# Kernel tuning notes

Measured on AMD Instinct MI355X. Metric: run time of the kernel, lower is better.

## Reference

```python
import jax, jax.numpy as jnp
import numpy as np

H = 20          # n_hidden
D_IN = 64       # max_len_input (encoder GRU input size)
VOCAB = 128     # decoder_dict_size
B = 8192
S = 128
MAX_DEC = 6


def _gru_cell(x, h, W_ih, W_hh, b_ih, b_hh):
    # PyTorch GRU cell: gates ordered [r, z, n]
    gi = x @ W_ih.T + b_ih
    gh = h @ W_hh.T + b_hh
    ir, iz, inn = jnp.split(gi, 3, axis=-1)
    hr, hz, hn = jnp.split(gh, 3, axis=-1)
    r = jax.nn.sigmoid(ir + hr)
    z = jax.nn.sigmoid(iz + hz)
    n = jnp.tanh(inn + r * hn)
    return (1.0 - z) * n + z * h


def setup_inputs() -> dict:
    key = jax.random.key(0)
    ks = jax.random.split(key, 32)
    s = 0.1
    p = {}
    p["x"] = jax.random.normal(ks[0], (B, S, D_IN), dtype=jnp.float32)
    # encoder GRU (2 layers)
    p["enc_Wih0"] = jax.random.normal(ks[1], (3 * H, D_IN)) * s
    p["enc_Whh0"] = jax.random.normal(ks[2], (3 * H, H)) * s
    p["enc_bih0"] = jax.random.normal(ks[3], (3 * H,)) * s
    p["enc_bhh0"] = jax.random.normal(ks[4], (3 * H,)) * s
    p["enc_Wih1"] = jax.random.normal(ks[5], (3 * H, H)) * s
    p["enc_Whh1"] = jax.random.normal(ks[6], (3 * H, H)) * s
    p["enc_bih1"] = jax.random.normal(ks[7], (3 * H,)) * s
    p["enc_bhh1"] = jax.random.normal(ks[8], (3 * H,)) * s
    # decoder GRU (2 layers, input size H)
    p["dec_Wih0"] = jax.random.normal(ks[9], (3 * H, H)) * s
    p["dec_Whh0"] = jax.random.normal(ks[10], (3 * H, H)) * s
    p["dec_bih0"] = jax.random.normal(ks[11], (3 * H,)) * s
    p["dec_bhh0"] = jax.random.normal(ks[12], (3 * H,)) * s
    p["dec_Wih1"] = jax.random.normal(ks[13], (3 * H, H)) * s
    p["dec_Whh1"] = jax.random.normal(ks[14], (3 * H, H)) * s
    p["dec_bih1"] = jax.random.normal(ks[15], (3 * H,)) * s
    p["dec_bhh1"] = jax.random.normal(ks[16], (3 * H,)) * s
    # embedding / attention / output heads
    p["emb"] = jax.random.normal(ks[17], (VOCAB, H)) * s
    p["q_W"] = jax.random.normal(ks[18], (H, H)) * s
    p["q_b"] = jax.random.normal(ks[19], (H,)) * s
    p["comb_W"] = jax.random.normal(ks[20], (H, 2 * H)) * s
    p["comb_b"] = jax.random.normal(ks[21], (H,)) * s
    p["out_W"] = jax.random.normal(ks[22], (VOCAB, H)) * s
    p["out_b"] = jax.random.normal(ks[23], (VOCAB,)) * s
    return p


def reference(x, enc_Wih0, enc_Whh0, enc_bih0, enc_bhh0,
              enc_Wih1, enc_Whh1, enc_bih1, enc_bhh1,
              dec_Wih0, dec_Whh0, dec_bih0, dec_bhh0,
              dec_Wih1, dec_Whh1, dec_bih1, dec_bhh1,
              emb, q_W, q_b, comb_W, comb_b, out_W, out_b):
    b = x.shape[0]
    h0 = jnp.zeros((b, H), x.dtype)
    h1 = jnp.zeros((b, H), x.dtype)

    def enc_step(carry, xt):
        c0, c1 = carry
        c0 = _gru_cell(xt, c0, enc_Wih0, enc_Whh0, enc_bih0, enc_bhh0)
        c1 = _gru_cell(c0, c1, enc_Wih1, enc_Whh1, enc_bih1, enc_bhh1)
        return (c0, c1), c1

    (h0, h1), enc_out = jax.lax.scan(enc_step, (h0, h1), jnp.swapaxes(x, 0, 1))
    encoded = jnp.swapaxes(enc_out, 0, 1)  # [B, S, H]

    vec_in = jnp.zeros((b,), dtype=jnp.int32)
    logits_list, attn_list = [], []
    d0, d1 = h0, h1  # hidden carried from encoder
    for _ in range(MAX_DEC):
        e = emb[vec_in]                                 # [B, H]
        d0 = _gru_cell(e, d0, dec_Wih0, dec_Whh0, dec_bih0, dec_bhh0)
        d1 = _gru_cell(d0, d1, dec_Wih1, dec_Whh1, dec_bih1, dec_bhh1)
        buf = d1                                        # decoder output at this step
        query = buf @ q_W.T + q_b                       # [B, H]
        scores = jnp.einsum('bh,bsh->bs', query, encoded)
        w = jax.nn.softmax(scores, axis=1)              # [B, S]
        a = jnp.einsum('bs,bsh->bh', w, encoded)        # attention context
        comb = jnp.concatenate([buf, a], axis=1) @ comb_W.T + comb_b
        logits = comb @ out_W.T + out_b                 # [B, VOCAB]
        logits_list.append(logits)
        attn_list.append(w)
        vec_in = jnp.argmax(logits, axis=1)
    vec_out = jnp.stack(logits_list, axis=1)            # [B, 6, VOCAB]
    hidden = jnp.stack([d0, d1], axis=0)                # [2, B, H]
    attention_weights = jnp.stack(attn_list, axis=0)    # [6, B, S]
    return vec_out, hidden, attention_weights
```

## Files before the change

### kernel.cpp

```cpp
#include <hip/hip_runtime.h>


#define HN 20
#define DIN 64
#define NVOCAB 128
#define NB 8192
#define NS 128
#define NDEC 6

#define HID_OFF (NB * NDEC * NVOCAB)
#define ATTN_OFF (HID_OFF + 2 * NB * HN)

__device__ __forceinline__ float sigf(float x) {
    return 1.0f / (1.0f + __expf(-x));
}

__global__ __launch_bounds__(512)
void enc_kernel(const float* __restrict__ x,
                const float* __restrict__ Wih0, const float* __restrict__ Whh0,
                const float* __restrict__ bih0, const float* __restrict__ bhh0,
                const float* __restrict__ Wih1, const float* __restrict__ Whh1,
                const float* __restrict__ bih1, const float* __restrict__ bhh1,
                float* __restrict__ enc, float* __restrict__ hf0,
                float* __restrict__ hf1)
{
    __shared__ __align__(16) float W0[60][68];
    __shared__ __align__(16) float U0[60][28];
    __shared__ __align__(16) float W1[60][28];
    __shared__ __align__(16) float U1[60][28];
    __shared__ float bi0[60], bh0[60], bi1[60], bh1[60];
    __shared__ __align__(16) float xs[2][8][68];
    __shared__ __align__(16) float h0s[8][24];
    __shared__ __align__(16) float h1s[8][24];
    __shared__ float gs[8][80];

    const int tid  = threadIdx.x;
    const int bloc = tid & 7;
    const int r    = tid >> 3;
    const int sb   = tid >> 6;
    const int si   = tid & 63;
    const int bid  = (int)blockIdx.x;
    const int gblk = (bid & 7) * 128 + (bid >> 3);
    const int b0   = gblk * 8;

    for (int idx = tid; idx < 60 * 64; idx += 512)
        W0[idx >> 6][idx & 63] = Wih0[idx];
    for (int idx = tid; idx < 60 * 20; idx += 512) {
        int rr = idx / 20, ii = idx % 20;
        U0[rr][ii] = Whh0[idx];
        W1[rr][ii] = Wih1[idx];
        U1[rr][ii] = Whh1[idx];
    }
    if (tid < 60) {
        bi0[tid] = bih0[tid]; bh0[tid] = bhh0[tid];
        bi1[tid] = bih1[tid]; bh1[tid] = bhh1[tid];
    }
    for (int idx = tid; idx < 8 * 24; idx += 512) {
        (&h0s[0][0])[idx] = 0.0f;
        (&h1s[0][0])[idx] = 0.0f;
    }
    xs[0][sb][si] = x[(b0 + sb) * (NS * DIN) + si];
    __syncthreads();

    int cur = 0;
    for (int t = 0; t < NS; ++t) {
        float pf = 0.0f;
        if (t + 1 < NS)
            pf = x[((b0 + sb) * NS + t + 1) * DIN + si];

        if (r < 60) {
            float ax = bi0[r], ah = bh0[r];
            #pragma unroll
            for (int i = 0; i < DIN; ++i) ax += W0[r][i] * xs[cur][bloc][i];
            #pragma unroll
            for (int i = 0; i < HN; ++i)  ah += U0[r][i] * h0s[bloc][i];
            if (r < 40) gs[bloc][r] = ax + ah;
            else { gs[bloc][r] = ax; gs[bloc][r + 20] = ah; }
        }
        __syncthreads();

        xs[cur ^ 1][sb][si] = pf;
        if (r < HN) {
            float rr = sigf(gs[bloc][r]);
            float z  = sigf(gs[bloc][20 + r]);
            float n  = tanhf(gs[bloc][40 + r] + rr * gs[bloc][60 + r]);
            float hnew = (1.0f - z) * n + z * h0s[bloc][r];
            h0s[bloc][r] = hnew;
            if (t == NS - 1) hf0[(b0 + bloc) * HN + r] = hnew;
        }
        __syncthreads();

        if (r < 60) {
            float ax = bi1[r], ah = bh1[r];
            #pragma unroll
            for (int i = 0; i < HN; ++i) ax += W1[r][i] * h0s[bloc][i];
            #pragma unroll
            for (int i = 0; i < HN; ++i) ah += U1[r][i] * h1s[bloc][i];
            if (r < 40) gs[bloc][r] = ax + ah;
            else { gs[bloc][r] = ax; gs[bloc][r + 20] = ah; }
        }
        __syncthreads();

        if (r < HN) {
            float rr = sigf(gs[bloc][r]);
            float z  = sigf(gs[bloc][20 + r]);
            float n  = tanhf(gs[bloc][40 + r] + rr * gs[bloc][60 + r]);
            float hnew = (1.0f - z) * n + z * h1s[bloc][r];
            h1s[bloc][r] = hnew;
            enc[(t * HN + r) * NB + b0 + bloc] = hnew;
            if (t == NS - 1) hf1[(b0 + bloc) * HN + r] = hnew;
        }
        __syncthreads();
        cur ^= 1;
    }
}

__global__ __launch_bounds__(512)
void dec_kernel(const float* __restrict__ dWih0, const float* __restrict__ dWhh0,
                const float* __restrict__ dbih0, const float* __restrict__ dbhh0,
                const float* __restrict__ dWih1, const float* __restrict__ dWhh1,
                const float* __restrict__ dbih1, const float* __restrict__ dbhh1,
                const float* __restrict__ emb,  const float* __restrict__ qW,
                const float* __restrict__ qb,   const float* __restrict__ combW,
                const float* __restrict__ combb, const float* __restrict__ outW,
                const float* __restrict__ outb,
                const float* __restrict__ enc, const float* __restrict__ hf0,
                const float* __restrict__ hf1, float* __restrict__ out)
{
    __shared__ __align__(16) float el[NS * 164];
    __shared__ float ssb[NS * 9];
    __shared__ float hd0[8][24], hd1[8][24];
    __shared__ float gsd[8][80];
    __shared__ float qs[8][24];
    __shared__ float combp[8][24];
    __shared__ float cxp[2][20][8];
    __shared__ float pm[8][8];
    __shared__ int   pi[8][8];
    __shared__ float Ms[8], Sv[8];
    __shared__ int   toks[8];

    const int tid  = threadIdx.x;
    const int bloc = tid & 7;
    const int r    = tid >> 3;
    const int wv   = tid >> 6;
    const int bid  = (int)blockIdx.x;
    const int gblk = (bid & 7) * 128 + (bid >> 3);
    const int b0   = gblk * 8;

    for (int idx = tid; idx < 8 * HN; idx += 512) {
        int bb = idx & 7, k = idx >> 3;
        hd0[bb][k] = hf0[(b0 + bb) * HN + k];
        hd1[bb][k] = hf1[(b0 + bb) * HN + k];
    }
    if (tid < 8) toks[tid] = 0;
    for (int idx = tid; idx < NS * HN * 2; idx += 512) {
        int tk = idx >> 1, q = idx & 1;
        int t = tk / HN, k = tk % HN;
        float4 v = *(const float4*)(enc + (size_t)tk * NB + b0 + 4 * q);
        *(float4*)(&el[t * 164 + k * 8 + 4 * q]) = v;
    }
    __syncthreads();

    for (int s = 0; s < NDEC; ++s) {
        if (r < 60) {
            const float* er = emb + toks[bloc] * HN;
            float ax = dbih0[r], ah = dbhh0[r];
            #pragma unroll
            for (int i = 0; i < HN; ++i) {
                ax += dWih0[r * HN + i] * er[i];
                ah += dWhh0[r * HN + i] * hd0[bloc][i];
            }
            if (r < 40) gsd[bloc][r] = ax + ah;
            else { gsd[bloc][r] = ax; gsd[bloc][r + 20] = ah; }
        }
        __syncthreads();
        if (r < HN) {
            float rr = sigf(gsd[bloc][r]);
            float z  = sigf(gsd[bloc][20 + r]);
            float n  = tanhf(gsd[bloc][40 + r] + rr * gsd[bloc][60 + r]);
            hd0[bloc][r] = (1.0f - z) * n + z * hd0[bloc][r];
        }
        __syncthreads();
        if (r < 60) {
            float ax = dbih1[r], ah = dbhh1[r];
            #pragma unroll
            for (int i = 0; i < HN; ++i) {
                ax += dWih1[r * HN + i] * hd0[bloc][i];
                ah += dWhh1[r * HN + i] * hd1[bloc][i];
            }
            if (r < 40) gsd[bloc][r] = ax + ah;
            else { gsd[bloc][r] = ax; gsd[bloc][r + 20] = ah; }
        }
        __syncthreads();
        if (r < HN) {
            float rr = sigf(gsd[bloc][r]);
            float z  = sigf(gsd[bloc][20 + r]);
            float n  = tanhf(gsd[bloc][40 + r] + rr * gsd[bloc][60 + r]);
            hd1[bloc][r] = (1.0f - z) * n + z * hd1[bloc][r];
        }
        __syncthreads();
        if (r < HN) {
            float a = qb[r];
            #pragma unroll
            for (int i = 0; i < HN; ++i) a += qW[r * HN + i] * hd1[bloc][i];
            qs[bloc][r] = a;
        } else if (r < 2 * HN) {
            int k = r - HN;
            float a = combb[k];
            #pragma unroll
            for (int i = 0; i < HN; ++i) a += combW[k * 2 * HN + i] * hd1[bloc][i];
            combp[bloc][k] = a;
        }
        __syncthreads();
        float s0 = 0.0f, s1 = 0.0f;
        #pragma unroll
        for (int k = 0; k < HN; ++k) {
            float q = qs[bloc][k];
            s0 += q * el[r * 164 + k * 8 + bloc];
            s1 += q * el[(64 + r) * 164 + k * 8 + bloc];
        }
        {
            float m = fmaxf(s0, s1);
            m = fmaxf(m, __shfl_xor(m, 8));
            m = fmaxf(m, __shfl_xor(m, 16));
            m = fmaxf(m, __shfl_xor(m, 32));
            if (((tid >> 3) & 7) == 0) pm[wv][bloc] = m;
        }
        __syncthreads();
        if (tid < 8) {
            float m = pm[0][tid];
            #pragma unroll
            for (int w2 = 1; w2 < 8; ++w2) m = fmaxf(m, pm[w2][tid]);
            Ms[tid] = m;
        }
        __syncthreads();
        float e0 = __expf(s0 - Ms[bloc]);
        float e1 = __expf(s1 - Ms[bloc]);
        ssb[r * 9 + bloc] = e0;
        ssb[(64 + r) * 9 + bloc] = e1;
        {
            float sm = e0 + e1;
            sm += __shfl_xor(sm, 8);
            sm += __shfl_xor(sm, 16);
            sm += __shfl_xor(sm, 32);
            if (((tid >> 3) & 7) == 0) pm[wv][bloc] = sm;
        }
        __syncthreads();
        if (tid < 8) {
            float sm = pm[0][tid];
            #pragma unroll
            for (int w2 = 1; w2 < 8; ++w2) sm += pm[w2][tid];
            Sv[tid] = 1.0f / sm;
        }
        __syncthreads();
        {
            int vb = wv, vt = tid & 63;
            float inv = Sv[vb];
            size_t abase = (size_t)ATTN_OFF + (size_t)s * NB * NS + (size_t)(b0 + vb) * NS;
            out[abase + vt]      = ssb[vt * 9 + vb] * inv;
            out[abase + vt + 64] = ssb[(vt + 64) * 9 + vb] * inv;
        }
        if (r < 2 * HN) {
            int k  = (r < HN) ? r : r - HN;
            int tb = (r < HN) ? 0 : 64;
            float acc = 0.0f;
            for (int u = 0; u < 64; ++u)
                acc += ssb[(tb + u) * 9 + bloc] * el[(tb + u) * 164 + k * 8 + bloc];
            cxp[(r < HN) ? 0 : 1][k][bloc] = acc * Sv[bloc];
        }
        __syncthreads();
        if (r < HN) {
            float a = combp[bloc][r];
            #pragma unroll
            for (int i = 0; i < HN; ++i)
                a += combW[r * 2 * HN + HN + i] * (cxp[0][i][bloc] + cxp[1][i][bloc]);
            combp[bloc][r] = a;
        }
        __syncthreads();
        {
            float lg0 = outb[r], lg1 = outb[64 + r];
            #pragma unroll
            for (int k = 0; k < HN; ++k) {
                float c = combp[bloc][k];
                lg0 += outW[r * HN + k] * c;
                lg1 += outW[(64 + r) * HN + k] * c;
            }
            ssb[r * 9 + bloc] = lg0;
            ssb[(64 + r) * 9 + bloc] = lg1;
            float bv = lg0; int bi2 = r;
            if (lg1 > bv) { bv = lg1; bi2 = 64 + r; }
            #pragma unroll
            for (int d = 8; d <= 32; d <<= 1) {
                float ov = __shfl_xor(bv, d);
                int   oi = __shfl_xor(bi2, d);
                if (ov > bv || (ov == bv && oi < bi2)) { bv = ov; bi2 = oi; }
            }
            if (((tid >> 3) & 7) == 0) { pm[wv][bloc] = bv; pi[wv][bloc] = bi2; }
        }
        __syncthreads();
        {
            int vb = wv, vt = tid & 63;
            size_t lbase = (size_t)(b0 + vb) * (NDEC * NVOCAB) + (size_t)s * NVOCAB;
            out[lbase + vt]      = ssb[vt * 9 + vb];
            out[lbase + vt + 64] = ssb[(vt + 64) * 9 + vb];
        }
        if (tid < 8) {
            float bv = pm[0][tid]; int bi2 = pi[0][tid];
            #pragma unroll
            for (int w2 = 1; w2 < 8; ++w2) {
                float ov = pm[w2][tid]; int oi = pi[w2][tid];
                if (ov > bv || (ov == bv && oi < bi2)) { bv = ov; bi2 = oi; }
            }
            toks[tid] = bi2;
        }
        __syncthreads();
    }

    for (int idx = tid; idx < 8 * HN; idx += 512) {
        int bb = idx & 7, k = idx >> 3;
        out[HID_OFF + (b0 + bb) * HN + k] = hd0[bb][k];
        out[HID_OFF + NB * HN + (b0 + bb) * HN + k] = hd1[bb][k];
    }
}

extern "C" void kernel_launch(void* const* d_in, const int* in_sizes, int n_in,
                              void* d_out, int out_size, void* d_ws, size_t ws_size,
                              hipStream_t stream)
{
    const float* x        = (const float*)d_in[0];
    const float* eWih0    = (const float*)d_in[1];
    const float* eWhh0    = (const float*)d_in[2];
    const float* ebih0    = (const float*)d_in[3];
    const float* ebhh0    = (const float*)d_in[4];
    const float* eWih1    = (const float*)d_in[5];
    const float* eWhh1    = (const float*)d_in[6];
    const float* ebih1    = (const float*)d_in[7];
    const float* ebhh1    = (const float*)d_in[8];
    const float* dWih0    = (const float*)d_in[9];
    const float* dWhh0    = (const float*)d_in[10];
    const float* dbih0    = (const float*)d_in[11];
    const float* dbhh0    = (const float*)d_in[12];
    const float* dWih1    = (const float*)d_in[13];
    const float* dWhh1    = (const float*)d_in[14];
    const float* dbih1    = (const float*)d_in[15];
    const float* dbhh1    = (const float*)d_in[16];
    const float* emb      = (const float*)d_in[17];
    const float* qW       = (const float*)d_in[18];
    const float* qb       = (const float*)d_in[19];
    const float* combW    = (const float*)d_in[20];
    const float* combb    = (const float*)d_in[21];
    const float* outW     = (const float*)d_in[22];
    const float* outb     = (const float*)d_in[23];

    const size_t need = ((size_t)NS * HN * NB + 2 * (size_t)NB * HN) * sizeof(float);
    if (ws_size < need) return;

    float* ws  = (float*)d_ws;
    float* enc = ws;
    float* hf0 = ws + (size_t)NS * HN * NB;
    float* hf1 = hf0 + (size_t)NB * HN;

    enc_kernel<<<1024, 512, 0, stream>>>(x, eWih0, eWhh0, ebih0, ebhh0,
                                         eWih1, eWhh1, ebih1, ebhh1,
                                         enc, hf0, hf1);
    dec_kernel<<<1024, 512, 0, stream>>>(dWih0, dWhh0, dbih0, dbhh0,
                                         dWih1, dWhh1, dbih1, dbhh1,
                                         emb, qW, qb, combW, combb, outW, outb,
                                         enc, hf0, hf1, (float*)d_out);
}
```

Before: 1.165 ms.

## Skew encoder GRU layers into one pipelined step; widen decoder blocks and stage weights in LDS

The encoder loop is software-pipelined: at iteration i it computes layer 0 for step i and layer 1 for step i-1 together, which cuts the barriers per timestep from four to two. The matvecs now use float4 LDS reads, and the gate buffers are transposed. The decoder runs 1024 threads per block with one score and one logit per thread, splits the context reduction into four chunks, and loads all weights into shared memory once. In exchange the kernels use more LDS, the launch bounds ask for higher occupancy, and the two encoder layers each do one extra iteration's worth of predicated work.

```diff
diff --git a/kernel.cpp b/kernel.cpp
--- a/kernel.cpp
+++ b/kernel.cpp
@@ -15,7 +15,7 @@
     return 1.0f / (1.0f + __expf(-x));
 }
 
-__global__ __launch_bounds__(512)
+__global__ __launch_bounds__(512, 8)
 void enc_kernel(const float* __restrict__ x,
                 const float* __restrict__ Wih0, const float* __restrict__ Whh0,
                 const float* __restrict__ bih0, const float* __restrict__ bhh0,
@@ -25,14 +25,15 @@
                 float* __restrict__ hf1)
 {
     __shared__ __align__(16) float W0[60][68];
-    __shared__ __align__(16) float U0[60][28];
-    __shared__ __align__(16) float W1[60][28];
-    __shared__ __align__(16) float U1[60][28];
+    __shared__ __align__(16) float U0[60][20];
+    __shared__ __align__(16) float W1[60][20];
+    __shared__ __align__(16) float U1[60][20];
     __shared__ float bi0[60], bh0[60], bi1[60], bh1[60];
-    __shared__ __align__(16) float xs[2][8][68];
+    __shared__ __align__(16) float xs[8][68];
     __shared__ __align__(16) float h0s[8][24];
     __shared__ __align__(16) float h1s[8][24];
-    __shared__ float gs[8][80];
+    __shared__ float gA[80][8];
+    __shared__ float gB[80][8];
 
     const int tid  = threadIdx.x;
     const int bloc = tid & 7;
@@ -46,10 +47,9 @@
     for (int idx = tid; idx < 60 * 64; idx += 512)
         W0[idx >> 6][idx & 63] = Wih0[idx];
     for (int idx = tid; idx < 60 * 20; idx += 512) {
-        int rr = idx / 20, ii = idx % 20;
-        U0[rr][ii] = Whh0[idx];
-        W1[rr][ii] = Wih1[idx];
-        U1[rr][ii] = Whh1[idx];
+        (&U0[0][0])[idx] = Whh0[idx];
+        (&W1[0][0])[idx] = Wih1[idx];
+        (&U1[0][0])[idx] = Whh1[idx];
     }
     if (tid < 60) {
         bi0[tid] = bih0[tid]; bh0[tid] = bhh0[tid];
@@ -59,63 +59,81 @@
         (&h0s[0][0])[idx] = 0.0f;
         (&h1s[0][0])[idx] = 0.0f;
     }
-    xs[0][sb][si] = x[(b0 + sb) * (NS * DIN) + si];
+    xs[sb][si] = x[(b0 + sb) * (NS * DIN) + si];
     __syncthreads();
 
-    int cur = 0;
-    for (int t = 0; t < NS; ++t) {
+    for (int i = 0; i <= NS; ++i) {
         float pf = 0.0f;
-        if (t + 1 < NS)
-            pf = x[((b0 + sb) * NS + t + 1) * DIN + si];
-
-        if (r < 60) {
-            float ax = bi0[r], ah = bh0[r];
-            #pragma unroll
-            for (int i = 0; i < DIN; ++i) ax += W0[r][i] * xs[cur][bloc][i];
-            #pragma unroll
-            for (int i = 0; i < HN; ++i)  ah += U0[r][i] * h0s[bloc][i];
-            if (r < 40) gs[bloc][r] = ax + ah;
-            else { gs[bloc][r] = ax; gs[bloc][r + 20] = ah; }
-        }
-        __syncthreads();
-
-        xs[cur ^ 1][sb][si] = pf;
+        const bool havepf = (i <= NS - 2);
+        if (havepf)
+            pf = x[((b0 + sb) * NS + i + 1) * DIN + si];
+
+        const bool g0 = (i < NS)  && (r < 60);
+        const bool g1 = (i >= 1)  && (r < 60);
+        if (g0) {
+            float ax = bi0[r];
+            #pragma unroll
+            for (int q = 0; q < 16; ++q) {
+                float4 wv = *(const float4*)(&W0[r][4 * q]);
+                float4 xv = *(const float4*)(&xs[bloc][4 * q]);
+                ax += wv.x * xv.x + wv.y * xv.y + wv.z * xv.z + wv.w * xv.w;
+            }
+            float ah = bh0[r];
+            #pragma unroll
+            for (int q = 0; q < 5; ++q) {
+                float4 uv = *(const float4*)(&U0[r][4 * q]);
+                float4 hv = *(const float4*)(&h0s[bloc][4 * q]);
+                ah += uv.x * hv.x + uv.y * hv.y + uv.z * hv.z + uv.w * hv.w;
+            }
+            if (r < 40) gA[r][bloc] = ax + ah;
+            else { gA[r][bloc] = ax; gA[r + 20][bloc] = ah; }
+        }
+        if (g1) {
+            float bx = bi1[r];
+            #pragma unroll
+            for (int q = 0; q < 5; ++q) {
+                float4 wv = *(const float4*)(&W1[r][4 * q]);
+                float4 hv = *(const float4*)(&h0s[bloc][4 * q]);
+                bx += wv.x * hv.x + wv.y * hv.y + wv.z * hv.z + wv.w * hv.w;
+            }
+            float bh = bh1[r];
+            #pragma unroll
+            for (int q = 0; q < 5; ++q) {
+                float4 uv = *(const float4*)(&U1[r][4 * q]);
+                float4 hv = *(const float4*)(&h1s[bloc][4 * q]);
+                bh += uv.x * hv.x + uv.y * hv.y + uv.z * hv.z + uv.w * hv.w;
+            }
+            if (r < 40) gB[r][bloc] = bx + bh;
+            else { gB[r][bloc] = bx; gB[r + 20][bloc] = bh; }
+        }
+        __syncthreads();
+
+        if (havepf) xs[sb][si] = pf;
         if (r < HN) {
-            float rr = sigf(gs[bloc][r]);
-            float z  = sigf(gs[bloc][20 + r]);
-            float n  = tanhf(gs[bloc][40 + r] + rr * gs[bloc][60 + r]);
-            float hnew = (1.0f - z) * n + z * h0s[bloc][r];
-            h0s[bloc][r] = hnew;
-            if (t == NS - 1) hf0[(b0 + bloc) * HN + r] = hnew;
-        }
-        __syncthreads();
-
-        if (r < 60) {
-            float ax = bi1[r], ah = bh1[r];
-            #pragma unroll
-            for (int i = 0; i < HN; ++i) ax += W1[r][i] * h0s[bloc][i];
-            #pragma unroll
-            for (int i = 0; i < HN; ++i) ah += U1[r][i] * h1s[bloc][i];
-            if (r < 40) gs[bloc][r] = ax + ah;
-            else { gs[bloc][r] = ax; gs[bloc][r + 20] = ah; }
-        }
-        __syncthreads();
-
-        if (r < HN) {
-            float rr = sigf(gs[bloc][r]);
-            float z  = sigf(gs[bloc][20 + r]);
-            float n  = tanhf(gs[bloc][40 + r] + rr * gs[bloc][60 + r]);
-            float hnew = (1.0f - z) * n + z * h1s[bloc][r];
-            h1s[bloc][r] = hnew;
-            enc[(t * HN + r) * NB + b0 + bloc] = hnew;
-            if (t == NS - 1) hf1[(b0 + bloc) * HN + r] = hnew;
-        }
-        __syncthreads();
-        cur ^= 1;
+            if (i < NS) {
+                float rr = sigf(gA[r][bloc]);
+                float z  = sigf(gA[20 + r][bloc]);
+                float n  = tanhf(gA[40 + r][bloc] + rr * gA[60 + r][bloc]);
+                float hnew = (1.0f - z) * n + z * h0s[bloc][r];
+                h0s[bloc][r] = hnew;
+                if (i == NS - 1) hf0[(b0 + bloc) * HN + r] = hnew;
+            }
+            if (i >= 1) {
+                int t1 = i - 1;
+                float rr = sigf(gB[r][bloc]);
+                float z  = sigf(gB[20 + r][bloc]);
+                float n  = tanhf(gB[40 + r][bloc] + rr * gB[60 + r][bloc]);
+                float hnew = (1.0f - z) * n + z * h1s[bloc][r];
+                h1s[bloc][r] = hnew;
+                enc[(t1 * HN + r) * NB + b0 + bloc] = hnew;
+                if (t1 == NS - 1) hf1[(b0 + bloc) * HN + r] = hnew;
+            }
+        }
+        __syncthreads();
     }
 }
 
-__global__ __launch_bounds__(512)
+__global__ __launch_bounds__(1024, 4)
 void dec_kernel(const float* __restrict__ dWih0, const float* __restrict__ dWhh0,
                 const float* __restrict__ dbih0, const float* __restrict__ dbhh0,
                 const float* __restrict__ dWih1, const float* __restrict__ dWhh1,
@@ -129,13 +147,21 @@
 {
     __shared__ __align__(16) float el[NS * 164];
     __shared__ float ssb[NS * 9];
+    __shared__ __align__(16) float Wih0s[60][20], Whh0s[60][20];
+    __shared__ __align__(16) float Wih1s[60][20], Whh1s[60][20];
+    __shared__ __align__(16) float qWs[20][20];
+    __shared__ __align__(16) float combWs[20][40];
+    __shared__ __align__(16) float outWs[128][20];
+    __shared__ __align__(16) float embs[128][20];
+    __shared__ float bi0s[60], bh0s[60], bi1s[60], bh1s[60];
+    __shared__ float qbs[20], cbbs[20], outbs[128];
     __shared__ float hd0[8][24], hd1[8][24];
-    __shared__ float gsd[8][80];
+    __shared__ float gsd[80][8];
     __shared__ float qs[8][24];
     __shared__ float combp[8][24];
-    __shared__ float cxp[2][20][8];
-    __shared__ float pm[8][8];
-    __shared__ int   pi[8][8];
+    __shared__ float cxp[4][20][8];
+    __shared__ float pm[16][8];
+    __shared__ int   pix[16][8];
     __shared__ float Ms[8], Sv[8];
     __shared__ int   toks[8];
 
@@ -147,13 +173,31 @@
     const int gblk = (bid & 7) * 128 + (bid >> 3);
     const int b0   = gblk * 8;
 
-    for (int idx = tid; idx < 8 * HN; idx += 512) {
+    for (int idx = tid; idx < 60 * 20; idx += 1024) {
+        (&Wih0s[0][0])[idx] = dWih0[idx];
+        (&Whh0s[0][0])[idx] = dWhh0[idx];
+        (&Wih1s[0][0])[idx] = dWih1[idx];
+        (&Whh1s[0][0])[idx] = dWhh1[idx];
+    }
+    for (int idx = tid; idx < 400; idx += 1024) (&qWs[0][0])[idx] = qW[idx];
+    for (int idx = tid; idx < 800; idx += 1024) (&combWs[0][0])[idx] = combW[idx];
+    for (int idx = tid; idx < 2560; idx += 1024) {
+        (&outWs[0][0])[idx] = outW[idx];
+        (&embs[0][0])[idx]  = emb[idx];
+    }
+    if (tid < 60) {
+        bi0s[tid] = dbih0[tid]; bh0s[tid] = dbhh0[tid];
+        bi1s[tid] = dbih1[tid]; bh1s[tid] = dbhh1[tid];
+    }
+    if (tid < 20) { qbs[tid] = qb[tid]; cbbs[tid] = combb[tid]; }
+    if (tid < 128) outbs[tid] = outb[tid];
+    for (int idx = tid; idx < 8 * HN; idx += 1024) {
         int bb = idx & 7, k = idx >> 3;
         hd0[bb][k] = hf0[(b0 + bb) * HN + k];
         hd1[bb][k] = hf1[(b0 + bb) * HN + k];
     }
     if (tid < 8) toks[tid] = 0;
-    for (int idx = tid; idx < NS * HN * 2; idx += 512) {
+    for (int idx = tid; idx < NS * HN * 2; idx += 1024) {
         int tk = idx >> 1, q = idx & 1;
         int t = tk / HN, k = tk % HN;
         float4 v = *(const float4*)(enc + (size_t)tk * NB + b0 + 4 * q);
@@ -163,152 +207,142 @@
 
     for (int s = 0; s < NDEC; ++s) {
         if (r < 60) {
-            const float* er = emb + toks[bloc] * HN;
-            float ax = dbih0[r], ah = dbhh0[r];
+            const float* er = &embs[toks[bloc]][0];
+            float ax = bi0s[r], ah = bh0s[r];
             #pragma unroll
             for (int i = 0; i < HN; ++i) {
-                ax += dWih0[r * HN + i] * er[i];
-                ah += dWhh0[r * HN + i] * hd0[bloc][i];
-            }
-            if (r < 40) gsd[bloc][r] = ax + ah;
-            else { gsd[bloc][r] = ax; gsd[bloc][r + 20] = ah; }
+                ax += Wih0s[r][i] * er[i];
+                ah += Whh0s[r][i] * hd0[bloc][i];
+            }
+            if (r < 40) gsd[r][bloc] = ax + ah;
+            else { gsd[r][bloc] = ax; gsd[r + 20][bloc] = ah; }
         }
         __syncthreads();
         if (r < HN) {
-            float rr = sigf(gsd[bloc][r]);
-            float z  = sigf(gsd[bloc][20 + r]);
-            float n  = tanhf(gsd[bloc][40 + r] + rr * gsd[bloc][60 + r]);
+            float rr = sigf(gsd[r][bloc]);
+            float z  = sigf(gsd[20 + r][bloc]);
+            float n  = tanhf(gsd[40 + r][bloc] + rr * gsd[60 + r][bloc]);
             hd0[bloc][r] = (1.0f - z) * n + z * hd0[bloc][r];
         }
         __syncthreads();
         if (r < 60) {
-            float ax = dbih1[r], ah = dbhh1[r];
+            float ax = bi1s[r], ah = bh1s[r];
             #pragma unroll
             for (int i = 0; i < HN; ++i) {
-                ax += dWih1[r * HN + i] * hd0[bloc][i];
-                ah += dWhh1[r * HN + i] * hd1[bloc][i];
-            }
-            if (r < 40) gsd[bloc][r] = ax + ah;
-            else { gsd[bloc][r] = ax; gsd[bloc][r + 20] = ah; }
+                ax += Wih1s[r][i] * hd0[bloc][i];
+                ah += Whh1s[r][i] * hd1[bloc][i];
+            }
+            if (r < 40) gsd[r][bloc] = ax + ah;
+            else { gsd[r][bloc] = ax; gsd[r + 20][bloc] = ah; }
         }
         __syncthreads();
         if (r < HN) {
-            float rr = sigf(gsd[bloc][r]);
-            float z  = sigf(gsd[bloc][20 + r]);
-            float n  = tanhf(gsd[bloc][40 + r] + rr * gsd[bloc][60 + r]);
+            float rr = sigf(gsd[r][bloc]);
+            float z  = sigf(gsd[20 + r][bloc]);
+            float n  = tanhf(gsd[40 + r][bloc] + rr * gsd[60 + r][bloc]);
             hd1[bloc][r] = (1.0f - z) * n + z * hd1[bloc][r];
         }
         __syncthreads();
         if (r < HN) {
-            float a = qb[r];
-            #pragma unroll
-            for (int i = 0; i < HN; ++i) a += qW[r * HN + i] * hd1[bloc][i];
+            float a = qbs[r];
+            #pragma unroll
+            for (int i = 0; i < HN; ++i) a += qWs[r][i] * hd1[bloc][i];
             qs[bloc][r] = a;
         } else if (r < 2 * HN) {
             int k = r - HN;
-            float a = combb[k];
-            #pragma unroll
-            for (int i = 0; i < HN; ++i) a += combW[k * 2 * HN + i] * hd1[bloc][i];
+            float a = cbbs[k];
+            #pragma unroll
+            for (int i = 0; i < HN; ++i) a += combWs[k][i] * hd1[bloc][i];
             combp[bloc][k] = a;
         }
         __syncthreads();
-        float s0 = 0.0f, s1 = 0.0f;
+        float sc = 0.0f;
         #pragma unroll
-        for (int k = 0; k < HN; ++k) {
-            float q = qs[bloc][k];
-            s0 += q * el[r * 164 + k * 8 + bloc];
-            s1 += q * el[(64 + r) * 164 + k * 8 + bloc];
-        }
+        for (int k = 0; k < HN; ++k)
+            sc += qs[bloc][k] * el[r * 164 + k * 8 + bloc];
         {
-            float m = fmaxf(s0, s1);
+            float m = sc;
             m = fmaxf(m, __shfl_xor(m, 8));
             m = fmaxf(m, __shfl_xor(m, 16));
             m = fmaxf(m, __shfl_xor(m, 32));
-            if (((tid >> 3) & 7) == 0) pm[wv][bloc] = m;
+            if ((tid & 63) < 8) pm[wv][bloc] = m;
         }
         __syncthreads();
         if (tid < 8) {
             float m = pm[0][tid];
             #pragma unroll
-            for (int w2 = 1; w2 < 8; ++w2) m = fmaxf(m, pm[w2][tid]);
+            for (int w2 = 1; w2 < 16; ++w2) m = fmaxf(m, pm[w2][tid]);
             Ms[tid] = m;
         }
         __syncthreads();
-        float e0 = __expf(s0 - Ms[bloc]);
-        float e1 = __expf(s1 - Ms[bloc]);
-        ssb[r * 9 + bloc] = e0;
-        ssb[(64 + r) * 9 + bloc] = e1;
+        float ev = __expf(sc - Ms[bloc]);
+        ssb[r * 9 + bloc] = ev;
         {
-            float sm = e0 + e1;
+            float sm = ev;
             sm += __shfl_xor(sm, 8);
             sm += __shfl_xor(sm, 16);
             sm += __shfl_xor(sm, 32);
-            if (((tid >> 3) & 7) == 0) pm[wv][bloc] = sm;
+            if ((tid & 63) < 8) pm[wv][bloc] = sm;
         }
         __syncthreads();
         if (tid < 8) {
             float sm = pm[0][tid];
             #pragma unroll
-            for (int w2 = 1; w2 < 8; ++w2) sm += pm[w2][tid];
+            for (int w2 = 1; w2 < 16; ++w2) sm += pm[w2][tid];
             Sv[tid] = 1.0f / sm;
         }
         __syncthreads();
         {
-            int vb = wv, vt = tid & 63;
-            float inv = Sv[vb];
-            size_t abase = (size_t)ATTN_OFF + (size_t)s * NB * NS + (size_t)(b0 + vb) * NS;
-            out[abase + vt]      = ssb[vt * 9 + vb] * inv;
-            out[abase + vt + 64] = ssb[(vt + 64) * 9 + vb] * inv;
-        }
-        if (r < 2 * HN) {
-            int k  = (r < HN) ? r : r - HN;
-            int tb = (r < HN) ? 0 : 64;
+            int vb = tid >> 7, vt = tid & 127;
+            out[(size_t)ATTN_OFF + (size_t)s * NB * NS + (size_t)(b0 + vb) * NS + vt]
+                = ssb[vt * 9 + vb] * Sv[vb];
+        }
+        if (r < 80) {
+            int ch = r / 20, k = r - 20 * ch;
+            int t0 = ch * 32;
             float acc = 0.0f;
-            for (int u = 0; u < 64; ++u)
-                acc += ssb[(tb + u) * 9 + bloc] * el[(tb + u) * 164 + k * 8 + bloc];
-            cxp[(r < HN) ? 0 : 1][k][bloc] = acc * Sv[bloc];
+            for (int u = 0; u < 32; ++u)
+                acc += ssb[(t0 + u) * 9 + bloc] * el[(t0 + u) * 164 + k * 8 + bloc];
+            cxp[ch][k][bloc] = acc;
         }
         __syncthreads();
         if (r < HN) {
             float a = combp[bloc][r];
-            #pragma unroll
-            for (int i = 0; i < HN; ++i)
-                a += combW[r * 2 * HN + HN + i] * (cxp[0][i][bloc] + cxp[1][i][bloc]);
+            float inv = Sv[bloc];
+            #pragma unroll
+            for (int i = 0; i < HN; ++i) {
+                float cx = (cxp[0][i][bloc] + cxp[1][i][bloc]
+                          + cxp[2][i][bloc] + cxp[3][i][bloc]) * inv;
+                a += combWs[r][HN + i] * cx;
+            }
             combp[bloc][r] = a;
         }
         __syncthreads();
         {
-            float lg0 = outb[r], lg1 = outb[64 + r];
-            #pragma unroll
-            for (int k = 0; k < HN; ++k) {
-                float c = combp[bloc][k];
-                lg0 += outW[r * HN + k] * c;
-                lg1 += outW[(64 + r) * HN + k] * c;
-            }
-            ssb[r * 9 + bloc] = lg0;
-            ssb[(64 + r) * 9 + bloc] = lg1;
-            float bv = lg0; int bi2 = r;
-            if (lg1 > bv) { bv = lg1; bi2 = 64 + r; }
+            float lg = outbs[r];
+            #pragma unroll
+            for (int k = 0; k < HN; ++k) lg += outWs[r][k] * combp[bloc][k];
+            ssb[r * 9 + bloc] = lg;
+            float bv = lg; int bi2 = r;
             #pragma unroll
             for (int d = 8; d <= 32; d <<= 1) {
                 float ov = __shfl_xor(bv, d);
                 int   oi = __shfl_xor(bi2, d);
                 if (ov > bv || (ov == bv && oi < bi2)) { bv = ov; bi2 = oi; }
             }
-            if (((tid >> 3) & 7) == 0) { pm[wv][bloc] = bv; pi[wv][bloc] = bi2; }
+            if ((tid & 63) < 8) { pm[wv][bloc] = bv; pix[wv][bloc] = bi2; }
         }
         __syncthreads();
         {
-            int vb = wv, vt = tid & 63;
-            size_t lbase = (size_t)(b0 + vb) * (NDEC * NVOCAB) + (size_t)s * NVOCAB;
-            out[lbase + vt]      = ssb[vt * 9 + vb];
-            out[lbase + vt + 64] = ssb[(vt + 64) * 9 + vb];
+            int vb = tid >> 7, vt = tid & 127;
+            out[(size_t)(b0 + vb) * (NDEC * NVOCAB) + s * NVOCAB + vt]
+                = ssb[vt * 9 + vb];
         }
         if (tid < 8) {
-            float bv = pm[0][tid]; int bi2 = pi[0][tid];
-            #pragma unroll
-            for (int w2 = 1; w2 < 8; ++w2) {
-                float ov = pm[w2][tid]; int oi = pi[w2][tid];
+            float bv = pm[0][tid]; int bi2 = pix[0][tid];
+            #pragma unroll
+            for (int w2 = 1; w2 < 16; ++w2) {
+                float ov = pm[w2][tid]; int oi = pix[w2][tid];
                 if (ov > bv || (ov == bv && oi < bi2)) { bv = ov; bi2 = oi; }
             }
             toks[tid] = bi2;
@@ -316,7 +350,7 @@
         __syncthreads();
     }
 
-    for (int idx = tid; idx < 8 * HN; idx += 512) {
+    for (int idx = tid; idx < 8 * HN; idx += 1024) {
         int bb = idx & 7, k = idx >> 3;
         out[HID_OFF + (b0 + bb) * HN + k] = hd0[bb][k];
         out[HID_OFF + NB * HN + (b0 + bb) * HN + k] = hd1[bb][k];
@@ -363,8 +397,8 @@
     enc_kernel<<<1024, 512, 0, stream>>>(x, eWih0, eWhh0, ebih0, ebhh0,
                                          eWih1, eWhh1, ebih1, ebhh1,
                                          enc, hf0, hf1);
-    dec_kernel<<<1024, 512, 0, stream>>>(dWih0, dWhh0, dbih0, dbhh0,
-                                         dWih1, dWhh1, dbih1, dbhh1,
-                                         emb, qW, qb, combW, combb, outW, outb,
-                                         enc, hf0, hf1, (float*)d_out);
+    dec_kernel<<<1024, 1024, 0, stream>>>(dWih0, dWhh0, dbih0, dbhh0,
+                                          dWih1, dWhh1, dbih1, dbhh1,
+                                          emb, qW, qb, combW, combb, outW, outb,
+                                          enc, hf0, hf1, (float*)d_out);
 }
```

New measurement: 1.092 ms. -6.2%, faster.
